# Kernel optimization log

Hardware: AMD Instinct MI355X
Metric: run time of the kernel (lower is better)

The kernel has to match this reference:

```python
import jax, jax.numpy as jnp
import numpy as np

B, N, E, D, H, HW, L = 16, 32, 256, 256, 8, 784, 4
DH = D // H
FF = 4 * D
BN = B * N
BE = B * E
SCALE = 1.0 / np.sqrt(DH)


def _ln(x, g, b):
    m = x.mean(-1, keepdims=True)
    v = ((x - m) ** 2).mean(-1, keepdims=True)
    return (x - m) * jax.lax.rsqrt(v + 1e-5) * g + b


def setup_inputs() -> dict:
    key = jax.random.key(0)
    ks = iter(jax.random.split(key, 64))
    def w(shape, s=0.05):
        return jax.random.normal(next(ks), shape, jnp.float32) * s
    inp = {
        'nodes': w((B, N, D), 1.0),
        'edges': w((B, E, D), 1.0),
        'images': w((B, HW, D), 1.0),
        'mask': jnp.zeros((B * H, N + E, HW), jnp.float32),
        'node_enc': w((BN, D), 1.0),
        'edge_enc': w((BE, D), 1.0),
        'ln1_g': jnp.ones((L, D), jnp.float32), 'ln1_b': jnp.zeros((L, D), jnp.float32),
        'Wqkv': w((L, D, 3 * D)), 'bqkv': jnp.zeros((L, 3 * D), jnp.float32),
        'Wo': w((L, D, D)), 'bo': jnp.zeros((L, D), jnp.float32),
        'ls1': jnp.full((L, D), 0.1, jnp.float32),
        'ln2_g': jnp.ones((L, D), jnp.float32), 'ln2_b': jnp.zeros((L, D), jnp.float32),
        'Wn1': w((L, D, D)), 'bn1': jnp.zeros((L, D), jnp.float32),
        'Wn2': w((L, D, D)), 'bn2': jnp.zeros((L, D), jnp.float32),
        'We': w((L, D, D)), 'be': jnp.zeros((L, D), jnp.float32),
        'attn_p': w((L, H, DH), 1.0),
        'Weo': w((L, D, D)), 'beo': jnp.zeros((L, D), jnp.float32),
        'Wno': w((L, D, D)), 'bno': jnp.zeros((L, D), jnp.float32),
        'ls2': jnp.full((L, D), 0.1, jnp.float32),
        'ln3_g': jnp.ones((L, D), jnp.float32), 'ln3_b': jnp.zeros((L, D), jnp.float32),
        'W1': w((L, D, FF)), 'b1': jnp.zeros((L, FF), jnp.float32),
        'W2': w((L, FF, D)), 'b2': jnp.zeros((L, D), jnp.float32),
        'ls3': jnp.full((L, D), 0.1, jnp.float32),
        'edge_index': jax.random.randint(next(ks), (2, BE), 0, BN, jnp.int32),
    }
    return inp


def reference(nodes, edges, images, mask, node_enc, edge_enc,
              ln1_g, ln1_b, Wqkv, bqkv, Wo, bo, ls1,
              ln2_g, ln2_b, Wn1, bn1, Wn2, bn2, We, be, attn_p, Weo, beo, Wno, bno, ls2,
              ln3_g, ln3_b, W1, b1, W2, b2, ls3, edge_index):
    idx0, idx1 = edge_index[0], edge_index[1]
    ne = jnp.concatenate([nodes, edges], axis=1)  # [B, N+E, D]
    mask4 = mask.reshape(B, H, N + E, HW)
    for l in range(L):
        # cross-attention ne -> images
        ne1n = _ln(ne, ln1_g[l], ln1_b[l])
        q = (ne1n @ Wqkv[l, :, :D] + bqkv[l, :D]).reshape(B, N + E, H, DH)
        k = (images @ Wqkv[l, :, D:2 * D] + bqkv[l, D:2 * D]).reshape(B, HW, H, DH)
        v = (images @ Wqkv[l, :, 2 * D:] + bqkv[l, 2 * D:]).reshape(B, HW, H, DH)
        scores = jnp.einsum('bqhd,bkhd->bhqk', q, k) * SCALE + mask4
        attn = jax.nn.softmax(scores, axis=-1)
        ctx = jnp.einsum('bhqk,bkhd->bqhd', attn, v).reshape(B, N + E, D)
        ne1 = ne + ls1[l] * (ctx @ Wo[l] + bo[l])
        # modified GAT on flattened graph
        ne2n = _ln(ne1, ln2_g[l], ln2_b[l])
        nodes_f = ne2n[:, :N].reshape(BN, D) + node_enc
        edges_f = ne2n[:, N:].reshape(BE, D) + edge_enc
        fn = (nodes_f @ Wn1[l] + bn1[l])[idx0]
        sn = (nodes_f @ Wn2[l] + bn2[l])[idx0]  # NOTE: original code uses edge_index[0] here too
        ep = edges_f @ We[l] + be[l]
        hidden = jax.nn.gelu(fn + sn + ep, approximate=False)  # [BE, D]
        pres = (hidden.reshape(BE, H, DH) * attn_p[l]).sum(-1)  # [BE, H]
        mseg = jax.ops.segment_max(pres, idx0, num_segments=BN)
        expv = jnp.exp(pres - mseg[idx0])
        denom = jax.ops.segment_sum(expv, idx0, num_segments=BN)
        alpha = expv / denom[idx0]  # scatter_softmax over destination nodes
        new_edges = hidden @ Weo[l] + beo[l]
        vals = (nodes_f[idx1] + new_edges) @ Wno[l] + bno[l]
        vals = vals.reshape(BE, H, DH) * alpha[..., None]
        new_nodes = jax.ops.segment_sum(vals.reshape(BE, D), idx0, num_segments=BN)
        gat = jnp.concatenate([new_nodes.reshape(B, N, D), new_edges.reshape(B, E, D)], axis=1)
        ne2 = ne1 + ls2[l] * gat
        # FFN
        ne3n = _ln(ne2, ln3_g[l], ln3_b[l])
        ffn = jax.nn.gelu(ne3n @ W1[l] + b1[l], approximate=False) @ W2[l] + b2[l]
        ne = ne2 + ls3[l] * ffn
    return ne
```

## Files before the change

kernel.cpp:

```cpp
#include <hip/hip_runtime.h>
#include <math.h>

static constexpr int B_  = 16;
static constexpr int N_  = 32;
static constexpr int E_  = 256;
static constexpr int D_  = 256;
static constexpr int H_  = 8;
static constexpr int HW_ = 784;
static constexpr int L_  = 4;
static constexpr int DH_ = 32;
static constexpr int FF_ = 1024;
static constexpr int BN_ = 512;
static constexpr int BE_ = 4096;
static constexpr int NE_ = 288;
static constexpr int NC_ = 13;
static constexpr int NBLK_ = B_ * H_ * 9;
static constexpr size_t KVSZ_ = (size_t)B_ * HW_ * 512;
#define SCALE_ 0.17677669529663687f

static constexpr size_t LAYER_W = 1114112;
static constexpr size_t OFF_Q   = 0;
static constexpr size_t OFF_WO  = 196608;
static constexpr size_t OFF_WN1 = 262144;
static constexpr size_t OFF_WE  = 393216;
static constexpr size_t OFF_WEO = 458752;
static constexpr size_t OFF_WNO = 524288;
static constexpr size_t OFF_W1  = 589824;
static constexpr size_t OFF_W2  = 851968;

typedef __attribute__((ext_vector_type(8))) short bf16x8;
typedef __attribute__((ext_vector_type(4))) float f32x4;

typedef __attribute__((address_space(1))) const unsigned int gas_uint;
typedef __attribute__((address_space(3))) unsigned int las_uint;

__device__ __forceinline__ void gload16(const unsigned short* g, unsigned short* lds) {
    __builtin_amdgcn_global_load_lds((gas_uint*)g, (las_uint*)lds, 16, 0, 0);
}

__device__ __forceinline__ float gelu_f(float x) {
    return 0.5f * x * (1.0f + erff(x * 0.7071067811865476f));
}

__device__ __forceinline__ unsigned short f2bf(float x) {
    unsigned u = __float_as_uint(x);
    u += 0x7FFFu + ((u >> 16) & 1u);
    return (unsigned short)(u >> 16);
}
__device__ __forceinline__ unsigned pack2bf(float a, float b) {
    return (unsigned)f2bf(a) | ((unsigned)f2bf(b) << 16);
}
__device__ __forceinline__ float bf2f(unsigned short u) {
    return __uint_as_float(((unsigned)u) << 16);
}


__global__ void concat_kernel(const float* __restrict__ nodes, const float* __restrict__ edges,
                              float* __restrict__ ne) {
    int tid = blockIdx.x * 256 + threadIdx.x;
    int d = tid & 255;
    int row = tid >> 8;
    int b = row / NE_, pos = row % NE_;
    float v = (pos < N_) ? nodes[(size_t)(b * N_ + pos) * D_ + d]
                         : edges[(size_t)(b * E_ + (pos - N_)) * D_ + d];
    ne[tid] = v;
}

__global__ void zeroinit_kernel(int* maskflag) {
    if (threadIdx.x == 0 && blockIdx.x == 0) *maskflag = 0;
}

__global__ __launch_bounds__(256) void maskchk_kernel(const float* __restrict__ mask,
                                                      int* __restrict__ flag) {
    const size_t total = (size_t)B_ * H_ * NE_ * HW_ / 4;
    const uint4* m = (const uint4*)mask;
    unsigned acc = 0;
    for (size_t i = (size_t)blockIdx.x * 256 + threadIdx.x; i < total; i += (size_t)gridDim.x * 256) {
        uint4 v = m[i];
        acc |= v.x | v.y | v.z | v.w;
    }
    unsigned long long bal = __ballot(acc != 0);
    if (bal != 0 && (threadIdx.x & 63) == (__ffsll((long long)bal) - 1))
        atomicOr(flag, 1);
}

__global__ __launch_bounds__(128) void premask_kernel(const float* __restrict__ mask,
                                                      unsigned short* __restrict__ pmask,
                                                      const int* __restrict__ flag) {
    if (*flag == 0) return;
    const int bid = blockIdx.x;
    const int c = bid % NC_;
    const int bq = bid / NC_;
    const int h = bq & 7;
    const int qt = (bq >> 3) % 9;
    const int b = (bq >> 3) / 9;
    const int q0 = qt * 32, c0 = c * 64;
    __shared__ float ts[32][68];
    const int t = threadIdx.x;
    const int row = t >> 2, cg = (t & 3) * 16;
    const float* mrow = mask + ((size_t)(b * H_ + h) * NE_ + q0 + row) * (size_t)HW_;
    #pragma unroll
    for (int i = 0; i < 4; ++i) {
        int col = c0 + cg + i * 4;
        float4 m4;
        if (col + 4 <= HW_) {
            m4 = *(const float4*)(mrow + col);
        } else {
            m4.x = (col + 0 < HW_) ? mrow[col + 0] : -1e30f;
            m4.y = (col + 1 < HW_) ? mrow[col + 1] : -1e30f;
            m4.z = (col + 2 < HW_) ? mrow[col + 2] : -1e30f;
            m4.w = (col + 3 < HW_) ? mrow[col + 3] : -1e30f;
        }
        *(float4*)&ts[row][cg + i * 4] = m4;
    }
    __syncthreads();
    const int w = t >> 6, lg = (t & 63) >> 4, lr = t & 15;
    const int r0 = w * 16 + lg * 4;
    unsigned u[8];
    #pragma unroll
    for (int rg = 0; rg < 4; ++rg) {
        u[rg * 2 + 0] = pack2bf(ts[r0 + rg][0 * 16 + lr], ts[r0 + rg][1 * 16 + lr]);
        u[rg * 2 + 1] = pack2bf(ts[r0 + rg][2 * 16 + lr], ts[r0 + rg][3 * 16 + lr]);
    }
    uint4* dst = (uint4*)(pmask + (size_t)bid * 2048 + t * 16);
    dst[0] = make_uint4(u[0], u[1], u[2], u[3]);
    dst[1] = make_uint4(u[4], u[5], u[6], u[7]);
}

__device__ __forceinline__ float ln_from_val(float v, int d,
                                             const float* __restrict__ g, const float* __restrict__ bta,
                                             float* sh1, float* sh2) {
    float s = v, s2 = v * v;
    #pragma unroll
    for (int o = 32; o >= 1; o >>= 1) { s += __shfl_down(s, o); s2 += __shfl_down(s2, o); }
    int lane = d & 63, w = d >> 6;
    if (lane == 0) { sh1[w] = s; sh2[w] = s2; }
    __syncthreads();
    if (d == 0) {
        float a = sh1[0] + sh1[1] + sh1[2] + sh1[3];
        float c = sh2[0] + sh2[1] + sh2[2] + sh2[3];
        sh1[0] = a; sh2[0] = c;
    }
    __syncthreads();
    float mean = sh1[0] * (1.0f / D_);
    float var  = sh2[0] * (1.0f / D_) - mean * mean;
    float rstd = rsqrtf(var + 1e-5f);
    return (v - mean) * rstd * g[d] + bta[d];
}

__global__ __launch_bounds__(256) void ln_kernel(const float* __restrict__ x,
                                                 unsigned short* __restrict__ y,
                                                 const float* __restrict__ g,
                                                 const float* __restrict__ bta) {
    __shared__ float sh1[4], sh2[4];
    const int row = blockIdx.x, d = threadIdx.x;
    float v = x[(size_t)row * D_ + d];
    y[(size_t)row * D_ + d] = f2bf(ln_from_val(v, d, g, bta, sh1, sh2));
}

__global__ __launch_bounds__(256) void ln2enc_kernel(const float* __restrict__ x,
                                                     const float* __restrict__ g,
                                                     const float* __restrict__ bta,
                                                     const float* __restrict__ node_enc,
                                                     const float* __restrict__ edge_enc,
                                                     unsigned short* __restrict__ nodes_f,
                                                     unsigned short* __restrict__ edges_f) {
    __shared__ float sh1[4], sh2[4];
    const int row = blockIdx.x, d = threadIdx.x;
    float v = x[(size_t)row * D_ + d];
    float val = ln_from_val(v, d, g, bta, sh1, sh2);
    int b = row / NE_, pos = row % NE_;
    if (pos < N_) {
        int rn = b * N_ + pos;
        nodes_f[(size_t)rn * D_ + d] = f2bf(val + node_enc[(size_t)rn * D_ + d]);
    } else {
        int re = b * E_ + (pos - N_);
        edges_f[(size_t)re * D_ + d] = f2bf(val + edge_enc[(size_t)re * D_ + d]);
    }
}

__global__ __launch_bounds__(256) void gatagg_ln_kernel(
    const float* __restrict__ vals, const float* __restrict__ pres,
    const int* __restrict__ csr_off, const int* __restrict__ csr_perm,
    const float* __restrict__ new_edges, const float* __restrict__ ls2l,
    const float* __restrict__ g, const float* __restrict__ bta,
    float* __restrict__ ne, unsigned short* __restrict__ lnb) {
    __shared__ float sh1[4], sh2[4];
    __shared__ float sms[8], sden[8];
    const int row = blockIdx.x, d = threadIdx.x;
    int b = row / NE_, pos = row % NE_;
    float gv;
    if (pos < N_) {
        int n = b * N_ + pos;
        int s = csr_off[n], e2 = csr_off[n + 1];
        if (d < 8) {
            float mx = -INFINITY;
            for (int i = s; i < e2; ++i) mx = fmaxf(mx, pres[csr_perm[i] * H_ + d]);
            float sum = 0.f;
            for (int i = s; i < e2; ++i) sum += __expf(pres[csr_perm[i] * H_ + d] - mx);
            sms[d] = mx; sden[d] = sum;
        }
        __syncthreads();
        int h = d >> 5;
        float ms = sms[h];
        float rd = 1.0f / sden[h];
        float acc = 0.f;
        for (int i = s; i < e2; ++i) {
            int e = csr_perm[i];
            acc += vals[(size_t)e * D_ + d] * (__expf(pres[e * H_ + h] - ms) * rd);
        }
        gv = acc;
    } else {
        gv = new_edges[(size_t)(b * E_ + (pos - N_)) * D_ + d];
    }
    float v = ne[(size_t)row * D_ + d] + ls2l[d] * gv;
    ne[(size_t)row * D_ + d] = v;
    lnb[(size_t)row * D_ + d] = f2bf(ln_from_val(v, d, g, bta, sh1, sh2));
}

__global__ __launch_bounds__(256) void wtrans_kernel(
    const float* __restrict__ Wqkv, const float* __restrict__ Wo,
    const float* __restrict__ Wn1,  const float* __restrict__ Wn2,
    const float* __restrict__ We,   const float* __restrict__ Weo,
    const float* __restrict__ Wno,  const float* __restrict__ W1,
    const float* __restrict__ W2,   unsigned short* __restrict__ wT,
    unsigned short* __restrict__ kvwT)
{
    const int bid = blockIdx.x;
    const int l = bid / 1088;
    int tl = bid % 1088;
    const float* src; int ld, K, Nn; unsigned short* dst;
    if (tl < 576) {
        int mid = tl >> 6; tl &= 63;
        K = 256; Nn = 256;
        if (mid == 0) {
            src = Wqkv + (size_t)l * 256 * 768; ld = 768;
            dst = wT + (size_t)l * LAYER_W + OFF_Q;
        } else if (mid < 3) {
            src = Wqkv + (size_t)l * 256 * 768 + mid * 256; ld = 768;
            dst = kvwT + ((size_t)l * 512 + (size_t)(mid - 1) * 256) * 256;
        } else {
            const float* bases[6] = {Wo, Wn1, Wn2, We, Weo, Wno};
            src = bases[mid - 3] + (size_t)l * 65536; ld = 256;
            dst = wT + (size_t)l * LAYER_W + OFF_WO + (size_t)(mid - 3) * 65536;
        }
    } else if (tl < 832) {
        tl -= 576; K = 256; Nn = 1024;
        src = W1 + (size_t)l * 262144; ld = 1024;
        dst = wT + (size_t)l * LAYER_W + OFF_W1;
    } else {
        tl -= 832; K = 1024; Nn = 256;
        src = W2 + (size_t)l * 262144; ld = 256;
        dst = wT + (size_t)l * LAYER_W + OFF_W2;
    }
    const int ntn = Nn >> 5;
    const int k0 = (tl / ntn) << 5, n0 = (tl % ntn) << 5;
    __shared__ float ts[32][33];
    const int t = threadIdx.x;
    const int kl = t >> 5, nl = t & 31;
    #pragma unroll
    for (int rr = 0; rr < 4; ++rr)
        ts[kl + rr * 8][nl] = src[(size_t)(k0 + kl + rr * 8) * ld + n0 + nl];
    __syncthreads();
    const int onl = t >> 3, okl = (t & 7) << 2;
    ushort4 o;
    o.x = f2bf(ts[okl + 0][onl]); o.y = f2bf(ts[okl + 1][onl]);
    o.z = f2bf(ts[okl + 2][onl]); o.w = f2bf(ts[okl + 3][onl]);
    *(ushort4*)&dst[(size_t)(n0 + onl) * K + k0 + okl] = o;
}


struct GArgs {
    const unsigned short* A;
    const unsigned short* Bt;
    const float* bias;
    const float* bias2;
    void* C;
    int lda, ldc, K, outbf, nbx;
};

template<int MODE, int OUTBF>
__global__ __launch_bounds__(256) void mgemm_kernel(
    const unsigned short* __restrict__ A, int lda,
    const unsigned short* __restrict__ Bt,
    const float* __restrict__ bias,
    const float* __restrict__ bias2,
    const float* __restrict__ res,
    const float* __restrict__ ls,
    void* __restrict__ Cv, int ldc, int K)
{
    __shared__ __align__(16) unsigned short As[64 * 64];
    __shared__ __align__(16) unsigned short Bs[64 * 64];
    const int m0 = blockIdx.y * 64, n0 = blockIdx.x * 64;
    const int t = threadIdx.x;
    const int l = t & 63, w = t >> 6;
    const int wr = (w >> 1) * 32, wc = (w & 1) * 32;
    const int frow = l & 15, kg = l >> 4;
    const int srow = w * 8 + (l >> 3);
    const int scolh = 8 * ((l & 7) ^ (l >> 3));
    const int ldsoff = w * 512;
    const int sw = (frow & 7) << 3;
    f32x4 acc[2][2];
    acc[0][0] = (f32x4){0.f,0.f,0.f,0.f}; acc[0][1] = acc[0][0];
    acc[1][0] = acc[0][0];                acc[1][1] = acc[0][0];
    for (int k0 = 0; k0 < K; k0 += 64) {
        const unsigned short* ga = A  + (size_t)(m0 + srow) * lda + k0 + scolh;
        const unsigned short* gb = Bt + (size_t)(n0 + srow) * K   + k0 + scolh;
        gload16(ga,                As + ldsoff);
        gload16(ga + 32 * lda,     As + ldsoff + 2048);
        gload16(gb,                Bs + ldsoff);
        gload16(gb + (size_t)32 * K, Bs + ldsoff + 2048);
        __syncthreads();
        #pragma unroll
        for (int kk = 0; kk < 2; ++kk) {
            const int off = (kk * 32 + kg * 8) ^ sw;
            bf16x8 af0 = *(const bf16x8*)&As[(wr + frow) * 64 + off];
            bf16x8 af1 = *(const bf16x8*)&As[(wr + 16 + frow) * 64 + off];
            bf16x8 bf0 = *(const bf16x8*)&Bs[(wc + frow) * 64 + off];
            bf16x8 bf1 = *(const bf16x8*)&Bs[(wc + 16 + frow) * 64 + off];
            acc[0][0] = __builtin_amdgcn_mfma_f32_16x16x32_bf16(af0, bf0, acc[0][0], 0, 0, 0);
            acc[0][1] = __builtin_amdgcn_mfma_f32_16x16x32_bf16(af0, bf1, acc[0][1], 0, 0, 0);
            acc[1][0] = __builtin_amdgcn_mfma_f32_16x16x32_bf16(af1, bf0, acc[1][0], 0, 0, 0);
            acc[1][1] = __builtin_amdgcn_mfma_f32_16x16x32_bf16(af1, bf1, acc[1][1], 0, 0, 0);
        }
        __syncthreads();
    }
    #pragma unroll
    for (int fr = 0; fr < 2; ++fr) {
        #pragma unroll
        for (int fc = 0; fc < 2; ++fc) {
            int n = n0 + wc + fc * 16 + frow;
            float bv = (bias2 != nullptr && n >= 256) ? bias2[n - 256] : bias[n];
            float lv = (MODE == 2) ? ls[n] : 0.f;
            #pragma unroll
            for (int rg = 0; rg < 4; ++rg) {
                int m = m0 + wr + fr * 16 + kg * 4 + rg;
                float vv = acc[fr][fc][rg] + bv;
                if (MODE == 1) vv = gelu_f(vv);
                if (MODE == 2) vv = res[(size_t)m * ldc + n] + lv * vv;
                if (OUTBF) ((unsigned short*)Cv)[(size_t)m * ldc + n] = f2bf(vv);
                else       ((float*)Cv)[(size_t)m * ldc + n] = vv;
            }
        }
    }
}

__global__ __launch_bounds__(256) void mgemm_weo_kernel(
    const unsigned short* __restrict__ A,
    const unsigned short* __restrict__ Bt,
    const float* __restrict__ bias,
    const unsigned short* __restrict__ nodes_f,
    const int* __restrict__ idx1,
    float* __restrict__ new_edges,
    unsigned short* __restrict__ vin)
{
    __shared__ __align__(16) unsigned short As[64 * 64];
    __shared__ __align__(16) unsigned short Bs[64 * 64];
    const int m0 = blockIdx.y * 64, n0 = blockIdx.x * 64;
    const int t = threadIdx.x;
    const int l = t & 63, w = t >> 6;
    const int wr = (w >> 1) * 32, wc = (w & 1) * 32;
    const int frow = l & 15, kg = l >> 4;
    const int srow = w * 8 + (l >> 3);
    const int scolh = 8 * ((l & 7) ^ (l >> 3));
    const int ldsoff = w * 512;
    const int sw = (frow & 7) << 3;
    f32x4 acc[2][2];
    acc[0][0] = (f32x4){0.f,0.f,0.f,0.f}; acc[0][1] = acc[0][0];
    acc[1][0] = acc[0][0];                acc[1][1] = acc[0][0];
    for (int k0 = 0; k0 < 256; k0 += 64) {
        const unsigned short* ga = A  + (size_t)(m0 + srow) * 256 + k0 + scolh;
        const unsigned short* gb = Bt + (size_t)(n0 + srow) * 256 + k0 + scolh;
        gload16(ga,                 As + ldsoff);
        gload16(ga + 32 * 256,      As + ldsoff + 2048);
        gload16(gb,                 Bs + ldsoff);
        gload16(gb + 32 * 256,      Bs + ldsoff + 2048);
        __syncthreads();
        #pragma unroll
        for (int kk = 0; kk < 2; ++kk) {
            const int off = (kk * 32 + kg * 8) ^ sw;
            bf16x8 af0 = *(const bf16x8*)&As[(wr + frow) * 64 + off];
            bf16x8 af1 = *(const bf16x8*)&As[(wr + 16 + frow) * 64 + off];
            bf16x8 bf0 = *(const bf16x8*)&Bs[(wc + frow) * 64 + off];
            bf16x8 bf1 = *(const bf16x8*)&Bs[(wc + 16 + frow) * 64 + off];
            acc[0][0] = __builtin_amdgcn_mfma_f32_16x16x32_bf16(af0, bf0, acc[0][0], 0, 0, 0);
            acc[0][1] = __builtin_amdgcn_mfma_f32_16x16x32_bf16(af0, bf1, acc[0][1], 0, 0, 0);
            acc[1][0] = __builtin_amdgcn_mfma_f32_16x16x32_bf16(af1, bf0, acc[1][0], 0, 0, 0);
            acc[1][1] = __builtin_amdgcn_mfma_f32_16x16x32_bf16(af1, bf1, acc[1][1], 0, 0, 0);
        }
        __syncthreads();
    }
    #pragma unroll
    for (int fr = 0; fr < 2; ++fr) {
        #pragma unroll
        for (int rg = 0; rg < 4; ++rg) {
            int m = m0 + wr + fr * 16 + kg * 4 + rg;
            int src = idx1[m];
            #pragma unroll
            for (int fc = 0; fc < 2; ++fc) {
                int n = n0 + wc + fc * 16 + frow;
                float vv = acc[fr][fc][rg] + bias[n];
                new_edges[(size_t)m * 256 + n] = vv;
                vin[(size_t)m * 256 + n] = f2bf(bf2f(nodes_f[(size_t)src * 256 + n]) + vv);
            }
        }
    }
}

__global__ __launch_bounds__(256) void mgemm2_kernel(GArgs g0, GArgs g1, int nblk0) {
    const bool first = (int)blockIdx.x < nblk0;
    GArgs g = first ? g0 : g1;
    const int bid = first ? blockIdx.x : blockIdx.x - nblk0;
    __shared__ __align__(16) unsigned short As[64 * 64];
    __shared__ __align__(16) unsigned short Bs[64 * 64];
    const int m0 = (bid / g.nbx) * 64, n0 = (bid % g.nbx) * 64;
    const int t = threadIdx.x;
    const int l = t & 63, w = t >> 6;
    const int wr = (w >> 1) * 32, wc = (w & 1) * 32;
    const int frow = l & 15, kg = l >> 4;
    const int srow = w * 8 + (l >> 3);
    const int scolh = 8 * ((l & 7) ^ (l >> 3));
    const int ldsoff = w * 512;
    const int sw = (frow & 7) << 3;
    f32x4 acc[2][2];
    acc[0][0] = (f32x4){0.f,0.f,0.f,0.f}; acc[0][1] = acc[0][0];
    acc[1][0] = acc[0][0];                acc[1][1] = acc[0][0];
    for (int k0 = 0; k0 < g.K; k0 += 64) {
        const unsigned short* ga = g.A  + (size_t)(m0 + srow) * g.lda + k0 + scolh;
        const unsigned short* gb = g.Bt + (size_t)(n0 + srow) * g.K   + k0 + scolh;
        gload16(ga,                  As + ldsoff);
        gload16(ga + 32 * g.lda,     As + ldsoff + 2048);
        gload16(gb,                  Bs + ldsoff);
        gload16(gb + (size_t)32 * g.K, Bs + ldsoff + 2048);
        __syncthreads();
        #pragma unroll
        for (int kk = 0; kk < 2; ++kk) {
            const int off = (kk * 32 + kg * 8) ^ sw;
            bf16x8 af0 = *(const bf16x8*)&As[(wr + frow) * 64 + off];
            bf16x8 af1 = *(const bf16x8*)&As[(wr + 16 + frow) * 64 + off];
            bf16x8 bf0 = *(const bf16x8*)&Bs[(wc + frow) * 64 + off];
            bf16x8 bf1 = *(const bf16x8*)&Bs[(wc + 16 + frow) * 64 + off];
            acc[0][0] = __builtin_amdgcn_mfma_f32_16x16x32_bf16(af0, bf0, acc[0][0], 0, 0, 0);
            acc[0][1] = __builtin_amdgcn_mfma_f32_16x16x32_bf16(af0, bf1, acc[0][1], 0, 0, 0);
            acc[1][0] = __builtin_amdgcn_mfma_f32_16x16x32_bf16(af1, bf0, acc[1][0], 0, 0, 0);
            acc[1][1] = __builtin_amdgcn_mfma_f32_16x16x32_bf16(af1, bf1, acc[1][1], 0, 0, 0);
        }
        __syncthreads();
    }
    #pragma unroll
    for (int fr = 0; fr < 2; ++fr) {
        #pragma unroll
        for (int fc = 0; fc < 2; ++fc) {
            int n = n0 + wc + fc * 16 + frow;
            float bv = (g.bias2 != nullptr && n >= 256) ? g.bias2[n - 256] : g.bias[n];
            #pragma unroll
            for (int rg = 0; rg < 4; ++rg) {
                int m = m0 + wr + fr * 16 + kg * 4 + rg;
                float vv = acc[fr][fc][rg] + bv;
                if (g.outbf) ((unsigned short*)g.C)[(size_t)m * g.ldc + n] = f2bf(vv);
                else         ((float*)g.C)[(size_t)m * g.ldc + n] = vv;
            }
        }
    }
}

template<int MODE>
__global__ __launch_bounds__(256) void mgemm128_kernel(
    const unsigned short* __restrict__ A, int lda,
    const unsigned short* __restrict__ Bt,
    const float* __restrict__ bias,
    unsigned short* __restrict__ C, int ldc, int K, int nbx)
{
    __shared__ __align__(16) unsigned short As[128 * 64];
    __shared__ __align__(16) unsigned short Bs[128 * 64];
    const int bid = blockIdx.x;
    const int m0 = (bid / nbx) * 128, n0 = (bid % nbx) * 128;
    const int t = threadIdx.x;
    const int l = t & 63, w = t >> 6;
    const int wr = (w >> 1) * 64, wc = (w & 1) * 64;
    const int frow = l & 15, kg = l >> 4;
    const int srow = w * 8 + (l >> 3);
    const int scolh = 8 * ((l & 7) ^ (l >> 3));
    const int ldsoff = w * 512;
    const int sw = (frow & 7) << 3;
    f32x4 acc[4][4];
    #pragma unroll
    for (int i = 0; i < 4; ++i)
        #pragma unroll
        for (int j = 0; j < 4; ++j) acc[i][j] = (f32x4){0.f, 0.f, 0.f, 0.f};
    for (int k0 = 0; k0 < K; k0 += 64) {
        #pragma unroll
        for (int j = 0; j < 4; ++j) {
            gload16(A  + (size_t)(m0 + j * 32 + srow) * lda + k0 + scolh, As + j * 2048 + ldsoff);
            gload16(Bt + (size_t)(n0 + j * 32 + srow) * K   + k0 + scolh, Bs + j * 2048 + ldsoff);
        }
        __syncthreads();
        #pragma unroll
        for (int kk = 0; kk < 2; ++kk) {
            const int off = (kk * 32 + kg * 8) ^ sw;
            bf16x8 af[4], bf[4];
            #pragma unroll
            for (int i = 0; i < 4; ++i) {
                af[i] = *(const bf16x8*)&As[(wr + i * 16 + frow) * 64 + off];
                bf[i] = *(const bf16x8*)&Bs[(wc + i * 16 + frow) * 64 + off];
            }
            #pragma unroll
            for (int i = 0; i < 4; ++i)
                #pragma unroll
                for (int j = 0; j < 4; ++j)
                    acc[i][j] = __builtin_amdgcn_mfma_f32_16x16x32_bf16(af[i], bf[j], acc[i][j], 0, 0, 0);
        }
        __syncthreads();
    }
    #pragma unroll
    for (int fr = 0; fr < 4; ++fr) {
        #pragma unroll
        for (int fc = 0; fc < 4; ++fc) {
            int n = n0 + wc + fc * 16 + frow;
            float bv = bias[n];
            #pragma unroll
            for (int rg = 0; rg < 4; ++rg) {
                int m = m0 + wr + fr * 16 + kg * 4 + rg;
                float vv = acc[fr][fc][rg] + bv;
                if (MODE == 1) vv = gelu_f(vv);
                C[(size_t)m * ldc + n] = f2bf(vv);
            }
        }
    }
}

__global__ __launch_bounds__(256) void mgemmkv_kernel(
    const float* __restrict__ img,
    const unsigned short* __restrict__ kvwT,
    const float* __restrict__ bqkv,
    unsigned short* __restrict__ kvall)
{
    __shared__ __align__(16) unsigned short As[128 * 64];
    __shared__ __align__(16) unsigned short Bs[128 * 64];
    const int bid = blockIdx.x;
    const int m0 = (bid / 16) * 128, n0 = (bid % 16) * 128;
    const int t = threadIdx.x;
    const int l = t & 63, w = t >> 6;
    const int wr = (w >> 1) * 64, wc = (w & 1) * 64;
    const int frow = l & 15, kg = l >> 4;
    const int srow = w * 8 + (l >> 3);
    const int scolh = 8 * ((l & 7) ^ (l >> 3));
    const int ldsoff = w * 512;
    const int sw = (frow & 7) << 3;
    f32x4 acc[4][4];
    #pragma unroll
    for (int i = 0; i < 4; ++i)
        #pragma unroll
        for (int j = 0; j < 4; ++j) acc[i][j] = (f32x4){0.f, 0.f, 0.f, 0.f};
    for (int k0 = 0; k0 < 256; k0 += 64) {
        #pragma unroll
        for (int j = 0; j < 4; ++j)
            gload16(kvwT + (size_t)(n0 + j * 32 + srow) * 256 + k0 + scolh, Bs + j * 2048 + ldsoff);
        #pragma unroll
        for (int i = 0; i < 4; ++i) {
            int u = t + i * 256;
            int row = u >> 3, colh = (u & 7) * 8;
            const float* src = img + (size_t)(m0 + row) * 256 + k0 + colh;
            float4 a0 = *(const float4*)(src);
            float4 a1 = *(const float4*)(src + 4);
            int scol = colh ^ ((row & 7) * 8);
            *(uint4*)&As[row * 64 + scol] = make_uint4(pack2bf(a0.x, a0.y), pack2bf(a0.z, a0.w),
                                                       pack2bf(a1.x, a1.y), pack2bf(a1.z, a1.w));
        }
        __syncthreads();
        #pragma unroll
        for (int kk = 0; kk < 2; ++kk) {
            const int off = (kk * 32 + kg * 8) ^ sw;
            bf16x8 af[4], bf[4];
            #pragma unroll
            for (int i = 0; i < 4; ++i) {
                af[i] = *(const bf16x8*)&As[(wr + i * 16 + frow) * 64 + off];
                bf[i] = *(const bf16x8*)&Bs[(wc + i * 16 + frow) * 64 + off];
            }
            #pragma unroll
            for (int i = 0; i < 4; ++i)
                #pragma unroll
                for (int j = 0; j < 4; ++j)
                    acc[i][j] = __builtin_amdgcn_mfma_f32_16x16x32_bf16(af[i], bf[j], acc[i][j], 0, 0, 0);
        }
        __syncthreads();
    }
    #pragma unroll
    for (int fr = 0; fr < 4; ++fr) {
        #pragma unroll
        for (int fc = 0; fc < 4; ++fc) {
            int n = n0 + wc + fc * 16 + frow;
            int layer = n >> 9, nn = n & 511;
            float bv = bqkv[layer * 768 + 256 + nn];
            unsigned short* dst = kvall + (size_t)layer * KVSZ_ + nn;
            #pragma unroll
            for (int rg = 0; rg < 4; ++rg) {
                int m = m0 + wr + fr * 16 + kg * 4 + rg;
                dst[(size_t)m * 512] = f2bf(acc[fr][fc][rg] + bv);
            }
        }
    }
}

__global__ __launch_bounds__(128) void attn_kernel(
    const unsigned short* __restrict__ lnb, const unsigned short* __restrict__ wq,
    const float* __restrict__ bqkv_l,
    const unsigned short* __restrict__ kv,
    const unsigned short* __restrict__ pmask, const int* __restrict__ maskflag,
    unsigned short* __restrict__ ctx)
{
    const int bid = blockIdx.x;
    const int h = bid & 7;
    const int qt = (bid >> 3) % 9;
    const int b = (bid >> 3) / 9;
    const int q0 = qt * 32;
    const int t = threadIdx.x;
    const int w = t >> 6, l = t & 63;
    const int lr = l & 15, lg = l >> 4;
    const int hasmask = *maskflag;

    __shared__ unsigned short Ks[2][64][40];
    __shared__ unsigned short Vs[2][32][72];
    __shared__ unsigned short Pl[2][16][72];
    __shared__ unsigned short Qlds[2][16][40];

    const int kkey = t >> 1, kdh = (t & 1) * 16;
    const int vdh = (t & 7) * 4, vk0 = (t >> 3) * 2;
    const unsigned short* kbase = kv + ((size_t)b * HW_) * 512 + h * DH_;
    const unsigned short* vbase = kv + ((size_t)b * HW_) * 512 + 256 + h * DH_;
    const uint4* mbase = (const uint4*)(pmask + (size_t)bid * NC_ * 2048 + t * 16);

    uint4 kq0, kq1;
    ushort4 va[2], vb4[2];
    uint4 mc0 = make_uint4(0,0,0,0), mc1 = mc0, mn0 = mc0, mn1 = mc0;

    auto issue_kv = [&](int c0) {
        {
            int key = c0 + kkey;
            bool ok = key < HW_;
            const unsigned short* kp = kbase + (size_t)(ok ? key : 0) * 512 + kdh;
            kq0 = *(const uint4*)(kp);
            kq1 = *(const uint4*)(kp + 8);
            if (!ok) { kq0 = make_uint4(0,0,0,0); kq1 = kq0; }
        }
        #pragma unroll
        for (int r = 0; r < 2; ++r) {
            int key = c0 + vk0 + 32 * r;
            bool ok0 = key < HW_, ok1 = (key + 1) < HW_;
            const unsigned short* vp = vbase + (size_t)(ok0 ? key : 0) * 512 + vdh;
            va[r]  = *(const ushort4*)(vp);
            vb4[r] = *(const ushort4*)(vp + (ok1 ? 512 : 0));
            if (!ok0) va[r]  = make_ushort4(0,0,0,0);
            if (!ok1) vb4[r] = make_ushort4(0,0,0,0);
        }
    };
    auto write_kv = [&](int bufi) {
        *(uint4*)&Ks[bufi][kkey][kdh]     = kq0;
        *(uint4*)&Ks[bufi][kkey][kdh + 8] = kq1;
        #pragma unroll
        for (int r = 0; r < 2; ++r) {
            const unsigned short* a = (const unsigned short*)&va[r];
            const unsigned short* c = (const unsigned short*)&vb4[r];
            #pragma unroll
            for (int i = 0; i < 4; ++i)
                *(unsigned*)&Vs[bufi][vdh + i][vk0 + 32 * r] = (unsigned)a[i] | ((unsigned)c[i] << 16);
        }
    };

    issue_kv(0);
    if (hasmask) { mc0 = mbase[0]; mc1 = mbase[1]; }

    bf16x8 qfrag;
    {
        unsigned short* Aln = &Ks[0][0][0];
        unsigned short* Wqs = Aln + 32 * 136;
        const unsigned short* asrc = lnb + (size_t)(b * NE_ + q0) * 256;
        const unsigned short* wsrc = wq + (size_t)(h * DH_) * 256;
        f32x4 qa[2];
        qa[0] = (f32x4){0.f, 0.f, 0.f, 0.f}; qa[1] = qa[0];
        #pragma unroll
        for (int ph = 0; ph < 2; ++ph) {
            #pragma unroll
            for (int i = 0; i < 4; ++i) {
                int u = t + i * 128;
                int row = u >> 4, col = (u & 15) * 8;
                *(uint4*)&Aln[row * 136 + col] = *(const uint4*)&asrc[(size_t)row * 256 + ph * 128 + col];
                *(uint4*)&Wqs[row * 136 + col] = *(const uint4*)&wsrc[(size_t)row * 256 + ph * 128 + col];
            }
            __syncthreads();
            #pragma unroll
            for (int kk = 0; kk < 4; ++kk) {
                bf16x8 af = *(const bf16x8*)&Aln[(w * 16 + lr) * 136 + kk * 32 + lg * 8];
                #pragma unroll
                for (int fc = 0; fc < 2; ++fc) {
                    bf16x8 bf = *(const bf16x8*)&Wqs[(fc * 16 + lr) * 136 + kk * 32 + lg * 8];
                    qa[fc] = __builtin_amdgcn_mfma_f32_16x16x32_bf16(af, bf, qa[fc], 0, 0, 0);
                }
            }
            __syncthreads();
        }
        #pragma unroll
        for (int fc = 0; fc < 2; ++fc) {
            float bq = bqkv_l[h * DH_ + fc * 16 + lr];
            #pragma unroll
            for (int rg = 0; rg < 4; ++rg)
                Qlds[w][lg * 4 + rg][fc * 16 + lr] = f2bf(qa[fc][rg] + bq);
        }
        __syncthreads();
        qfrag = *(const bf16x8*)&Qlds[w][lr][lg * 8];
    }

    f32x4 oacc[2];
    oacc[0] = (f32x4){0.f, 0.f, 0.f, 0.f}; oacc[1] = oacc[0];
    float m_i[4] = {-INFINITY, -INFINITY, -INFINITY, -INFINITY};
    float l_i[4] = {0.f, 0.f, 0.f, 0.f};

    write_kv(0);
    if (hasmask) { mn0 = mbase[128]; mn1 = mbase[129]; }
    __syncthreads();

    for (int c = 0; c < NC_; ++c) {
        const int c0 = c * 64;
        const int cb = c & 1, nb = cb ^ 1;
        if (c + 1 < NC_) issue_kv(c0 + 64);

        f32x4 sacc[4];
        #pragma unroll
        for (int fc = 0; fc < 4; ++fc) {
            sacc[fc] = (f32x4){0.f, 0.f, 0.f, 0.f};
            bf16x8 kf = *(const bf16x8*)&Ks[cb][fc * 16 + lr][lg * 8];
            sacc[fc] = __builtin_amdgcn_mfma_f32_16x16x32_bf16(qfrag, kf, sacc[fc], 0, 0, 0);
        }
        float s[4][4];
        if (hasmask) {
            unsigned uw[8] = {mc0.x, mc0.y, mc0.z, mc0.w, mc1.x, mc1.y, mc1.z, mc1.w};
            #pragma unroll
            for (int rg = 0; rg < 4; ++rg) {
                s[0][rg] = sacc[0][rg] * SCALE_ + bf2f((unsigned short)(uw[rg * 2] & 0xffff));
                s[1][rg] = sacc[1][rg] * SCALE_ + bf2f((unsigned short)(uw[rg * 2] >> 16));
                s[2][rg] = sacc[2][rg] * SCALE_ + bf2f((unsigned short)(uw[rg * 2 + 1] & 0xffff));
                s[3][rg] = sacc[3][rg] * SCALE_ + bf2f((unsigned short)(uw[rg * 2 + 1] >> 16));
            }
            float mloc[4];
            #pragma unroll
            for (int rg = 0; rg < 4; ++rg)
                mloc[rg] = fmaxf(fmaxf(s[0][rg], s[1][rg]), fmaxf(s[2][rg], s[3][rg]));
            #pragma unroll
            for (int off = 1; off < 16; off <<= 1)
                #pragma unroll
                for (int rg = 0; rg < 4; ++rg)
                    mloc[rg] = fmaxf(mloc[rg], __shfl_xor(mloc[rg], off));
            float scl[4], lloc[4];
            #pragma unroll
            for (int rg = 0; rg < 4; ++rg) {
                float mn = fmaxf(m_i[rg], mloc[rg]);
                scl[rg] = __expf(m_i[rg] - mn);
                m_i[rg] = mn;
            }
            #pragma unroll
            for (int rg = 0; rg < 4; ++rg) {
                float acc = 0.f;
                #pragma unroll
                for (int fc = 0; fc < 4; ++fc) {
                    float p = __expf(s[fc][rg] - m_i[rg]);
                    s[fc][rg] = p;
                    acc += p;
                }
                lloc[rg] = acc;
            }
            #pragma unroll
            for (int off = 1; off < 16; off <<= 1)
                #pragma unroll
                for (int rg = 0; rg < 4; ++rg)
                    lloc[rg] += __shfl_xor(lloc[rg], off);
            #pragma unroll
            for (int rg = 0; rg < 4; ++rg) {
                l_i[rg] = l_i[rg] * scl[rg] + lloc[rg];
                oacc[0][rg] *= scl[rg];
                oacc[1][rg] *= scl[rg];
            }
        } else {
            const bool tailc = (c == NC_ - 1);
            float lloc[4] = {0.f, 0.f, 0.f, 0.f};
            #pragma unroll
            for (int fc = 0; fc < 4; ++fc) {
                float pad = (tailc && (c0 + fc * 16 + lr) >= HW_) ? -1e30f : 0.f;
                #pragma unroll
                for (int rg = 0; rg < 4; ++rg) {
                    float p = __expf(sacc[fc][rg] * SCALE_ + pad);
                    s[fc][rg] = p;
                    lloc[rg] += p;
                }
            }
            #pragma unroll
            for (int off = 1; off < 16; off <<= 1)
                #pragma unroll
                for (int rg = 0; rg < 4; ++rg)
                    lloc[rg] += __shfl_xor(lloc[rg], off);
            #pragma unroll
            for (int rg = 0; rg < 4; ++rg)
                l_i[rg] += lloc[rg];
        }

        #pragma unroll
        for (int fc = 0; fc < 4; ++fc)
            #pragma unroll
            for (int rg = 0; rg < 4; ++rg)
                Pl[w][lg * 4 + rg][fc * 16 + lr] = f2bf(s[fc][rg]);
        #pragma unroll
        for (int ks2 = 0; ks2 < 2; ++ks2) {
            bf16x8 pf = *(const bf16x8*)&Pl[w][lr][ks2 * 32 + lg * 8];
            #pragma unroll
            for (int d2 = 0; d2 < 2; ++d2) {
                bf16x8 vf = *(const bf16x8*)&Vs[cb][d2 * 16 + lr][ks2 * 32 + lg * 8];
                oacc[d2] = __builtin_amdgcn_mfma_f32_16x16x32_bf16(pf, vf, oacc[d2], 0, 0, 0);
            }
        }

        if (hasmask) {
            mc0 = mn0; mc1 = mn1;
            if (c + 2 < NC_) {
                mn0 = mbase[(c + 2) * 128];
                mn1 = mbase[(c + 2) * 128 + 1];
            }
        }
        if (c + 1 < NC_) {
            write_kv(nb);
            __syncthreads();
        }
    }

    unsigned short* cbase = ctx + ((size_t)(b * NE_ + q0 + w * 16 + lg * 4)) * D_ + h * DH_;
    #pragma unroll
    for (int rg = 0; rg < 4; ++rg) {
        float inv = 1.0f / l_i[rg];
        #pragma unroll
        for (int d2 = 0; d2 < 2; ++d2)
            cbase[(size_t)rg * D_ + d2 * 16 + lr] = f2bf(oacc[d2][rg] * inv);
    }
}


__global__ __launch_bounds__(256) void hidden_kernel(
    const float* __restrict__ gn12,
    unsigned short* __restrict__ hid, const int* __restrict__ idx0,
    const float* __restrict__ attn_p_l, float* __restrict__ pres) {
    int e = blockIdx.x;
    int d = threadIdx.x;
    int n = idx0[e];
    float x = bf2f(hid[(size_t)e * D_ + d]) + gn12[(size_t)n * 512 + d] + gn12[(size_t)n * 512 + 256 + d];
    float hv = gelu_f(x);
    hid[(size_t)e * D_ + d] = f2bf(hv);
    float pr = hv * attn_p_l[d];
    #pragma unroll
    for (int o = 1; o < 32; o <<= 1) pr += __shfl_xor(pr, o);
    if ((d & 31) == 0) pres[e * H_ + (d >> 5)] = pr;
}


__global__ __launch_bounds__(512) void csr_build_kernel(const int* __restrict__ idx0,
                                                        int* __restrict__ csr_off) {
    __shared__ int cnt[BN_];
    __shared__ int buf[BN_];
    int t = threadIdx.x;
    cnt[t] = 0;
    __syncthreads();
    #pragma unroll
    for (int i = 0; i < BE_ / 512; ++i)
        atomicAdd(&cnt[idx0[t + i * 512]], 1);
    __syncthreads();
    int c = cnt[t];
    buf[t] = c;
    __syncthreads();
    for (int o = 1; o < BN_; o <<= 1) {
        int add = (t >= o) ? buf[t - o] : 0;
        __syncthreads();
        buf[t] += add;
        __syncthreads();
    }
    csr_off[t] = buf[t] - c;
    if (t == BN_ - 1) csr_off[BN_] = buf[t];
}

__global__ __launch_bounds__(64) void csr_fill(const int* __restrict__ idx0,
                                               const int* __restrict__ csr_off,
                                               int* __restrict__ csr_perm) {
    int n = blockIdx.x;
    int lane = threadIdx.x;
    int w = csr_off[n];
    for (int c0 = 0; c0 < BE_; c0 += 64) {
        int e = c0 + lane;
        bool m = (idx0[e] == n);
        unsigned long long bal = __ballot(m);
        if (m) {
            int pre = __popcll(bal & ((1ull << lane) - 1ull));
            csr_perm[w + pre] = e;
        }
        w += __popcll(bal);
    }
}


static void launch_mgemm(hipStream_t s, int mode, int outbf,
                         const unsigned short* A, int lda, const unsigned short* Bt,
                         const float* bias, const float* bias2, const float* res, const float* ls,
                         void* C, int ldc, int M, int N, int K) {
    dim3 g(N / 64, M / 64);
    if (mode == 0) {
        if (outbf) mgemm_kernel<0,1><<<g, 256, 0, s>>>(A, lda, Bt, bias, bias2, res, ls, C, ldc, K);
        else       mgemm_kernel<0,0><<<g, 256, 0, s>>>(A, lda, Bt, bias, bias2, res, ls, C, ldc, K);
    } else if (mode == 1) {
        mgemm_kernel<1,1><<<g, 256, 0, s>>>(A, lda, Bt, bias, bias2, res, ls, C, ldc, K);
    } else {
        mgemm_kernel<2,0><<<g, 256, 0, s>>>(A, lda, Bt, bias, bias2, res, ls, C, ldc, K);
    }
}

extern "C" void kernel_launch(void* const* d_in, const int* in_sizes, int n_in,
                              void* d_out, int out_size, void* d_ws, size_t ws_size,
                              hipStream_t stream) {
    const float* nodes    = (const float*)d_in[0];
    const float* edges    = (const float*)d_in[1];
    const float* images   = (const float*)d_in[2];
    const float* mask     = (const float*)d_in[3];
    const float* node_enc = (const float*)d_in[4];
    const float* edge_enc = (const float*)d_in[5];
    const float* ln1_g = (const float*)d_in[6];
    const float* ln1_b = (const float*)d_in[7];
    const float* Wqkv  = (const float*)d_in[8];
    const float* bqkv  = (const float*)d_in[9];
    const float* Wo    = (const float*)d_in[10];
    const float* bo    = (const float*)d_in[11];
    const float* ls1   = (const float*)d_in[12];
    const float* ln2_g = (const float*)d_in[13];
    const float* ln2_b = (const float*)d_in[14];
    const float* Wn1   = (const float*)d_in[15];
    const float* bn1   = (const float*)d_in[16];
    const float* Wn2   = (const float*)d_in[17];
    const float* bn2   = (const float*)d_in[18];
    const float* We    = (const float*)d_in[19];
    const float* be    = (const float*)d_in[20];
    const float* attn_p= (const float*)d_in[21];
    const float* Weo   = (const float*)d_in[22];
    const float* beo   = (const float*)d_in[23];
    const float* Wno   = (const float*)d_in[24];
    const float* bno   = (const float*)d_in[25];
    const float* ls2   = (const float*)d_in[26];
    const float* ln3_g = (const float*)d_in[27];
    const float* ln3_b = (const float*)d_in[28];
    const float* W1    = (const float*)d_in[29];
    const float* b1    = (const float*)d_in[30];
    const float* W2    = (const float*)d_in[31];
    const float* b2    = (const float*)d_in[32];
    const float* ls3   = (const float*)d_in[33];
    const int*   edge_index = (const int*)d_in[34];
    const int* idx0 = edge_index;
    const int* idx1 = edge_index + BE_;

    float* ne = (float*)d_out;

    float* cur = (float*)d_ws;
    auto alloc = [&](size_t nfl) { float* p = cur; cur += nfl; return p; };
    auto allocbf = [&](size_t nbf) { float* p = cur; cur += (nbf + 1) / 2; return (unsigned short*)p; };

    unsigned short* lnbuf   = allocbf((size_t)B_ * NE_ * D_);
    unsigned short* kvall   = allocbf((size_t)L_ * KVSZ_);
    unsigned short* ffnh    = allocbf((size_t)B_ * NE_ * FF_);
    unsigned short* ctxb    = allocbf((size_t)B_ * NE_ * D_);
    unsigned short* nodes_f = allocbf((size_t)BN_ * D_);
    unsigned short* edges_f = allocbf((size_t)BE_ * D_);
    unsigned short* hid     = allocbf((size_t)BE_ * D_);
    unsigned short* vin     = allocbf((size_t)BE_ * D_);
    unsigned short* pmaskb  = allocbf((size_t)NBLK_ * NC_ * 2048);
    unsigned short* kvwT    = allocbf((size_t)L_ * 512 * 256);
    float* gn12     = alloc((size_t)BN_ * 512);
    float* pres     = alloc((size_t)BE_ * H_);
    float* new_edges= alloc((size_t)BE_ * D_);
    float* valsb    = alloc((size_t)BE_ * D_);
    int* csr_off  = (int*)cur; cur += BN_ + 4;
    int* csr_perm = (int*)cur; cur += BE_;
    int* maskflag = (int*)cur; cur += 4;
    cur = (float*)(((uintptr_t)cur + 255) & ~(uintptr_t)255);
    unsigned short* wT = (unsigned short*)cur;

    zeroinit_kernel<<<1, 64, 0, stream>>>(maskflag);
    maskchk_kernel<<<2048, 256, 0, stream>>>(mask, maskflag);
    wtrans_kernel<<<4 * 1088, 256, 0, stream>>>(Wqkv, Wo, Wn1, Wn2, We, Weo, Wno, W1, W2, wT, kvwT);
    premask_kernel<<<NBLK_ * NC_, 128, 0, stream>>>(mask, pmaskb, maskflag);
    csr_build_kernel<<<1, 512, 0, stream>>>(idx0, csr_off);
    csr_fill<<<BN_, 64, 0, stream>>>(idx0, csr_off, csr_perm);
    concat_kernel<<<(B_ * NE_ * D_) / 256, 256, 0, stream>>>(nodes, edges, ne);
    mgemmkv_kernel<<<(B_ * HW_ / 128) * 16, 256, 0, stream>>>(images, kvwT, bqkv, kvall);

    for (int l = 0; l < L_; ++l) {
        const unsigned short* wTl = wT + (size_t)l * LAYER_W;
        const float* bqkv_l = bqkv + (size_t)l * 3 * D_;

        ln_kernel<<<B_ * NE_, 256, 0, stream>>>(ne, lnbuf, ln1_g + l * D_, ln1_b + l * D_);
        attn_kernel<<<NBLK_, 128, 0, stream>>>(lnbuf, wTl + OFF_Q, bqkv_l,
                                               kvall + (size_t)l * KVSZ_, pmaskb, maskflag, ctxb);
        launch_mgemm(stream, 2, 0, ctxb, D_, wTl + OFF_WO, bo + l * D_, nullptr, ne, ls1 + l * D_,
                     ne, D_, B_ * NE_, D_, D_);

        ln2enc_kernel<<<B_ * NE_, 256, 0, stream>>>(ne, ln2_g + l * D_, ln2_b + l * D_,
                                                    node_enc, edge_enc, nodes_f, edges_f);
        {
            GArgs gn { nodes_f, wTl + OFF_WN1, bn1 + l * D_, bn2 + l * D_, gn12, 256, 512, 256, 0, 8 };
            GArgs ge { edges_f, wTl + OFF_WE,  be + l * D_,  nullptr,      hid,  256, 256, 256, 1, 4 };
            int nb0 = (BN_ / 64) * 8;
            int nb1 = (BE_ / 64) * 4;
            mgemm2_kernel<<<nb0 + nb1, 256, 0, stream>>>(gn, ge, nb0);
        }
        hidden_kernel<<<BE_, 256, 0, stream>>>(gn12, hid, idx0, attn_p + (size_t)l * H_ * DH_, pres);
        mgemm_weo_kernel<<<dim3(4, BE_ / 64), 256, 0, stream>>>(
            hid, wTl + OFF_WEO, beo + l * D_, nodes_f, idx1, new_edges, vin);
        launch_mgemm(stream, 0, 0, vin, D_, wTl + OFF_WNO, bno + l * D_, nullptr, nullptr, nullptr,
                     valsb, D_, BE_, D_, D_);
        gatagg_ln_kernel<<<B_ * NE_, 256, 0, stream>>>(valsb, pres, csr_off, csr_perm,
                                                       new_edges, ls2 + l * D_,
                                                       ln3_g + l * D_, ln3_b + l * D_, ne, lnbuf);

        mgemm128_kernel<1><<<(B_ * NE_ / 128) * (FF_ / 128), 256, 0, stream>>>(
            lnbuf, 256, wTl + OFF_W1, b1 + l * FF_, ffnh, FF_, 256, FF_ / 128);
        launch_mgemm(stream, 2, 0, ffnh, FF_, wTl + OFF_W2, b2 + l * D_, nullptr, ne, ls3 + l * D_,
                     ne, D_, B_ * NE_, D_, FF_);
    }
}
```

Baseline: 583.3 us.

## Fuse LayerNorm into residual GEMM epilogues with full-row tiles

Adds a GEMM kernel whose blocks own 32 full rows (all 256 output columns), so the epilogue can apply the residual scale-add and then compute the row LayerNorm in place. It replaces the Wo GEMM plus ln2enc kernel, and the W2 GEMM plus the next layer's ln1 kernel, with the first ln1 hoisted before the loop. This removes separate LN launches and an extra read of the residual stream per layer. The cost is fewer blocks (144) with a larger B tile per block, which may lower occupancy and GEMM efficiency compared with the previous tiled GEMM. On the last layer the fused kernel still computes an unused LN using layer-3 parameters.

New measurement: 603.2 us. 1.03x slower.

```diff
diff --git a/kernel.cpp b/kernel.cpp
--- a/kernel.cpp
+++ b/kernel.cpp
@@ -156,27 +156,6 @@
     const int row = blockIdx.x, d = threadIdx.x;
     float v = x[(size_t)row * D_ + d];
     y[(size_t)row * D_ + d] = f2bf(ln_from_val(v, d, g, bta, sh1, sh2));
-}
-
-__global__ __launch_bounds__(256) void ln2enc_kernel(const float* __restrict__ x,
-                                                     const float* __restrict__ g,
-                                                     const float* __restrict__ bta,
-                                                     const float* __restrict__ node_enc,
-                                                     const float* __restrict__ edge_enc,
-                                                     unsigned short* __restrict__ nodes_f,
-                                                     unsigned short* __restrict__ edges_f) {
-    __shared__ float sh1[4], sh2[4];
-    const int row = blockIdx.x, d = threadIdx.x;
-    float v = x[(size_t)row * D_ + d];
-    float val = ln_from_val(v, d, g, bta, sh1, sh2);
-    int b = row / NE_, pos = row % NE_;
-    if (pos < N_) {
-        int rn = b * N_ + pos;
-        nodes_f[(size_t)rn * D_ + d] = f2bf(val + node_enc[(size_t)rn * D_ + d]);
-    } else {
-        int re = b * E_ + (pos - N_);
-        edges_f[(size_t)re * D_ + d] = f2bf(val + edge_enc[(size_t)re * D_ + d]);
-    }
 }
 
 __global__ __launch_bounds__(256) void gatagg_ln_kernel(
@@ -524,6 +503,132 @@
                 float vv = acc[fr][fc][rg] + bv;
                 if (MODE == 1) vv = gelu_f(vv);
                 C[(size_t)m * ldc + n] = f2bf(vv);
+            }
+        }
+    }
+}
+
+template<int ENC>
+__global__ __launch_bounds__(256) void mgemm_rowln_kernel(
+    const unsigned short* __restrict__ A, int lda,
+    const unsigned short* __restrict__ Bt,
+    const float* __restrict__ bias,
+    const float* __restrict__ ls,
+    float* __restrict__ ne,
+    const float* __restrict__ g,
+    const float* __restrict__ bta,
+    const float* __restrict__ node_enc,
+    const float* __restrict__ edge_enc,
+    unsigned short* __restrict__ out0,
+    unsigned short* __restrict__ out1,
+    int K)
+{
+    __shared__ __align__(16) unsigned short As[32 * 64];
+    __shared__ __align__(16) unsigned short Bs[256 * 64];
+    __shared__ float rsum[4][32], rsq[4][32];
+    const int m0 = blockIdx.x * 32;
+    const int t = threadIdx.x;
+    const int l = t & 63, w = t >> 6;
+    const int wc = w * 64;
+    const int frow = l & 15, kg = l >> 4;
+    const int srow = w * 8 + (l >> 3);
+    const int scolh = 8 * ((l & 7) ^ (l >> 3));
+    const int ldsoff = w * 512;
+    const int sw = (frow & 7) << 3;
+    f32x4 acc[2][4];
+    #pragma unroll
+    for (int fr = 0; fr < 2; ++fr)
+        #pragma unroll
+        for (int fc = 0; fc < 4; ++fc) acc[fr][fc] = (f32x4){0.f, 0.f, 0.f, 0.f};
+    for (int k0 = 0; k0 < K; k0 += 64) {
+        gload16(A + (size_t)(m0 + srow) * lda + k0 + scolh, As + ldsoff);
+        #pragma unroll
+        for (int j = 0; j < 8; ++j)
+            gload16(Bt + (size_t)(j * 32 + srow) * K + k0 + scolh, Bs + j * 2048 + ldsoff);
+        __syncthreads();
+        #pragma unroll
+        for (int kk = 0; kk < 2; ++kk) {
+            const int off = (kk * 32 + kg * 8) ^ sw;
+            bf16x8 af[2], bf[4];
+            #pragma unroll
+            for (int fr = 0; fr < 2; ++fr)
+                af[fr] = *(const bf16x8*)&As[(fr * 16 + frow) * 64 + off];
+            #pragma unroll
+            for (int fc = 0; fc < 4; ++fc)
+                bf[fc] = *(const bf16x8*)&Bs[(wc + fc * 16 + frow) * 64 + off];
+            #pragma unroll
+            for (int fr = 0; fr < 2; ++fr)
+                #pragma unroll
+                for (int fc = 0; fc < 4; ++fc)
+                    acc[fr][fc] = __builtin_amdgcn_mfma_f32_16x16x32_bf16(af[fr], bf[fc], acc[fr][fc], 0, 0, 0);
+        }
+        __syncthreads();
+    }
+    float v[2][4][4];
+    #pragma unroll
+    for (int fr = 0; fr < 2; ++fr) {
+        #pragma unroll
+        for (int fc = 0; fc < 4; ++fc) {
+            int n = wc + fc * 16 + frow;
+            float bv = bias[n], lv = ls[n];
+            #pragma unroll
+            for (int rg = 0; rg < 4; ++rg) {
+                int m = m0 + fr * 16 + kg * 4 + rg;
+                float x = ne[(size_t)m * 256 + n] + lv * (acc[fr][fc][rg] + bv);
+                ne[(size_t)m * 256 + n] = x;
+                v[fr][fc][rg] = x;
+            }
+        }
+    }
+    #pragma unroll
+    for (int fr = 0; fr < 2; ++fr) {
+        #pragma unroll
+        for (int rg = 0; rg < 4; ++rg) {
+            float s = 0.f, s2 = 0.f;
+            #pragma unroll
+            for (int fc = 0; fc < 4; ++fc) {
+                float x = v[fr][fc][rg];
+                s += x; s2 += x * x;
+            }
+            #pragma unroll
+            for (int off = 1; off < 16; off <<= 1) {
+                s  += __shfl_xor(s, off);
+                s2 += __shfl_xor(s2, off);
+            }
+            if (frow == 0) {
+                int r = fr * 16 + kg * 4 + rg;
+                rsum[w][r] = s; rsq[w][r] = s2;
+            }
+        }
+    }
+    __syncthreads();
+    #pragma unroll
+    for (int fr = 0; fr < 2; ++fr) {
+        #pragma unroll
+        for (int rg = 0; rg < 4; ++rg) {
+            int r = fr * 16 + kg * 4 + rg;
+            int m = m0 + r;
+            float tot = rsum[0][r] + rsum[1][r] + rsum[2][r] + rsum[3][r];
+            float sq  = rsq[0][r] + rsq[1][r] + rsq[2][r] + rsq[3][r];
+            float mean = tot * (1.0f / 256.0f);
+            float var  = sq * (1.0f / 256.0f) - mean * mean;
+            float rstd = rsqrtf(var + 1e-5f);
+            #pragma unroll
+            for (int fc = 0; fc < 4; ++fc) {
+                int n = wc + fc * 16 + frow;
+                float lnv = (v[fr][fc][rg] - mean) * rstd * g[n] + bta[n];
+                if (ENC == 0) {
+                    out0[(size_t)m * 256 + n] = f2bf(lnv);
+                } else {
+                    int b = m / NE_, pos = m % NE_;
+                    if (pos < N_) {
+                        int rn = b * N_ + pos;
+                        out0[(size_t)rn * 256 + n] = f2bf(lnv + node_enc[(size_t)rn * 256 + n]);
+                    } else {
+                        int re = b * E_ + (pos - N_);
+                        out1[(size_t)re * 256 + n] = f2bf(lnv + edge_enc[(size_t)re * 256 + n]);
+                    }
+                }
             }
         }
     }
@@ -991,19 +1096,19 @@
     csr_fill<<<BN_, 64, 0, stream>>>(idx0, csr_off, csr_perm);
     concat_kernel<<<(B_ * NE_ * D_) / 256, 256, 0, stream>>>(nodes, edges, ne);
     mgemmkv_kernel<<<(B_ * HW_ / 128) * 16, 256, 0, stream>>>(images, kvwT, bqkv, kvall);
+    ln_kernel<<<B_ * NE_, 256, 0, stream>>>(ne, lnbuf, ln1_g, ln1_b);
 
     for (int l = 0; l < L_; ++l) {
         const unsigned short* wTl = wT + (size_t)l * LAYER_W;
         const float* bqkv_l = bqkv + (size_t)l * 3 * D_;
-
-        ln_kernel<<<B_ * NE_, 256, 0, stream>>>(ne, lnbuf, ln1_g + l * D_, ln1_b + l * D_);
+        const int lnx = (l + 1 < L_) ? (l + 1) : l;
+
         attn_kernel<<<NBLK_, 128, 0, stream>>>(lnbuf, wTl + OFF_Q, bqkv_l,
                                                kvall + (size_t)l * KVSZ_, pmaskb, maskflag, ctxb);
-        launch_mgemm(stream, 2, 0, ctxb, D_, wTl + OFF_WO, bo + l * D_, nullptr, ne, ls1 + l * D_,
-                     ne, D_, B_ * NE_, D_, D_);
-
-        ln2enc_kernel<<<B_ * NE_, 256, 0, stream>>>(ne, ln2_g + l * D_, ln2_b + l * D_,
-                                                    node_enc, edge_enc, nodes_f, edges_f);
+        mgemm_rowln_kernel<1><<<B_ * NE_ / 32, 256, 0, stream>>>(
+            ctxb, 256, wTl + OFF_WO, bo + l * D_, ls1 + l * D_, ne,
+            ln2_g + l * D_, ln2_b + l * D_, node_enc, edge_enc, nodes_f, edges_f, 256);
+
         {
             GArgs gn { nodes_f, wTl + OFF_WN1, bn1 + l * D_, bn2 + l * D_, gn12, 256, 512, 256, 0, 8 };
             GArgs ge { edges_f, wTl + OFF_WE,  be + l * D_,  nullptr,      hid,  256, 256, 256, 1, 4 };
@@ -1022,7 +1127,8 @@
 
         mgemm128_kernel<1><<<(B_ * NE_ / 128) * (FF_ / 128), 256, 0, stream>>>(
             lnbuf, 256, wTl + OFF_W1, b1 + l * FF_, ffnh, FF_, 256, FF_ / 128);
-        launch_mgemm(stream, 2, 0, ffnh, FF_, wTl + OFF_W2, b2 + l * D_, nullptr, ne, ls3 + l * D_,
-                     ne, D_, B_ * NE_, D_, FF_);
-    }
-}
+        mgemm_rowln_kernel<0><<<B_ * NE_ / 32, 256, 0, stream>>>(
+            ffnh, FF_, wTl + OFF_W2, b2 + l * D_, ls3 + l * D_, ne,
+            ln1_g + lnx * D_, ln1_b + lnx * D_, nullptr, nullptr, lnbuf, nullptr, FF_);
+    }
+}
```
